# Performance work log

Measured on AMD Instinct MI355X. Metric: run time of the kernel, lower is better.

Reference implementation:

```python
import jax, jax.numpy as jnp
import numpy as np

N = 50000; NE = 250000; NH_EDGES = 125000
DIN = 100; NHID = 100; HEADS = 2; NREL = 500; DREL = 100
ALPHA = 0.2; B = 65536


def l2norm(x, eps=1e-12):
    n = jnp.sqrt(jnp.sum(x * x, axis=1, keepdims=True))
    return x / jnp.maximum(n, eps)


def sp_att(x, edge, edge_embed, a, a2, concat):
    """KBGAT sparse graph attention layer (eval mode, no dropout).
    x: (N, din) node feats; edge: (2, E) int; edge_embed: (E, drel).
    a: (dout, 2*din + drel); a2: (dout,). Aggregates onto edge[0]."""
    din = x.shape[1]
    a_src, a_dst, a_rel = a[:, :din], a[:, din:2 * din], a[:, 2 * din:]
    # edge_m = a @ cat(x[src], x[dst], edge_embed).T, computed without the big concat
    edge_m = x[edge[0]] @ a_src.T + x[edge[1]] @ a_dst.T + edge_embed @ a_rel.T  # (E, dout)
    powers = -jax.nn.leaky_relu(edge_m @ a2, ALPHA)  # (E,)
    edge_e = jnp.exp(powers)
    rowsum = jax.ops.segment_sum(edge_e, edge[0], num_segments=x.shape[0])  # (N,)
    rowsum = jnp.where(rowsum == 0.0, jnp.asarray(1e-12, x.dtype), rowsum)
    h = jax.ops.segment_sum(edge_e[:, None] * edge_m, edge[0], num_segments=x.shape[0])  # (N, dout)
    h = h / rowsum[:, None]
    return jax.nn.elu(h) if concat else h


def setup_inputs() -> dict:
    key = jax.random.key(0)
    ks = jax.random.split(key, 16)
    s1 = np.sqrt(2.0 / (NHID + 2 * DIN + DREL)) * 1.414  # xavier-ish gains
    s2 = np.sqrt(2.0 / (HEADS * NHID + 3 * HEADS * NHID)) * 1.414
    return {
        "entity_embeddings": jax.random.normal(ks[0], (N, DIN), jnp.float32),
        "relation_embeddings": jax.random.normal(ks[1], (NREL, DREL), jnp.float32),
        "entity_rank": jax.random.normal(ks[2], (N,), jnp.float32),
        "a_heads": jax.random.normal(ks[3], (HEADS, NHID, 2 * DIN + DREL), jnp.float32) * s1,
        "a2_heads": jax.random.normal(ks[4], (HEADS, NHID), jnp.float32) * 0.1,
        "W_gat": jax.random.normal(ks[5], (DREL, HEADS * NHID), jnp.float32) * s2,
        "a_out": jax.random.normal(ks[6], (HEADS * NHID, 3 * HEADS * NHID), jnp.float32) * s2,
        "a2_out": jax.random.normal(ks[7], (HEADS * NHID,), jnp.float32) * 0.1,
        "W_entities": jax.random.normal(ks[8], (DIN, HEADS * NHID), jnp.float32) * s2,
        "edge_list": jax.random.randint(ks[9], (2, NE), 0, N, jnp.int32),
        "edge_type": jax.random.randint(ks[10], (NE,), 0, NREL, jnp.int32),
        "train_indices_nhop": jax.random.randint(ks[11], (NH_EDGES, 4), 0, NREL, jnp.int32),
        "batch_inputs": jax.random.randint(ks[12], (B, 3), 0, N, jnp.int32),
    }


def reference(entity_embeddings, relation_embeddings, entity_rank, a_heads, a2_heads,
              W_gat, a_out, a2_out, W_entities, edge_list, edge_type,
              train_indices_nhop, batch_inputs):
    # SpKBGATModified.forward, confidence=False path, eval mode (dropout off).
    x0 = l2norm(entity_embeddings)  # F.normalize(entity_embeddings, p=2, dim=1)
    # 2-hop edges: edge_list_nhop = [nhop[:,3]; nhop[:,0]], edge_type_nhop = nhop[:,1:3]
    edge_list_nhop = jnp.stack([train_indices_nhop[:, 3], train_indices_nhop[:, 0]], axis=0)
    edge_type_nhop = train_indices_nhop[:, 1:3]
    edge = jnp.concatenate([edge_list, edge_list_nhop], axis=1)  # (2, E_total)
    # first-layer edge relation embeddings
    ee1 = jnp.concatenate([
        relation_embeddings[edge_type],
        relation_embeddings[edge_type_nhop[:, 0]] + relation_embeddings[edge_type_nhop[:, 1]],
    ], axis=0)  # (E_total, DREL)
    # multi-head attention, concat heads along feature dim (head0 first, as torch.cat)
    heads = jax.vmap(lambda a, a2: sp_att(x0, edge, ee1, a, a2, True))(a_heads, a2_heads)  # (H, N, NHID)
    x = jnp.transpose(heads, (1, 0, 2)).reshape(x0.shape[0], HEADS * NHID)
    # relation projection and second-hop relation embeddings
    out_relation_1 = relation_embeddings @ W_gat  # (NREL, H*NHID)
    ee2 = jnp.concatenate([
        out_relation_1[edge_type],
        out_relation_1[edge_type_nhop[:, 0]] + out_relation_1[edge_type_nhop[:, 1]],
    ], axis=0)
    x = jax.nn.elu(sp_att(x, edge, ee2, a_out, a2_out, False))  # (N, H*NHID)
    # mask rows touched by batch tails, residual-update and renormalize
    mask = jnp.zeros((x0.shape[0],), x.dtype).at[batch_inputs[:, 2]].set(1.0)
    out_entity_1 = x0 @ W_entities + mask[:, None] * x
    out_entity_1 = l2norm(out_entity_1)
    return out_entity_1, out_relation_1
```

## Files before the change

### kernel.cpp

```cpp
#include <hip/hip_runtime.h>
#include <math.h>

#define NN    50000
#define MP    50048
#define NEDGE 250000
#define NHOPE 125000
#define ETOT  375000
#define NRELS 500
#define BATCH 65536
#define LB1   6250
#define HBMAX 5769

typedef __attribute__((ext_vector_type(8))) short bf16x8;
typedef __attribute__((ext_vector_type(4))) float f32x4;

__device__ __forceinline__ unsigned short bf16rne(float f) {
  unsigned u = __float_as_uint(f);
  unsigned r = (u + 0x7FFFu + ((u >> 16) & 1u)) >> 16;
  return (unsigned short)r;
}
__device__ __forceinline__ float b2f(unsigned short u) {
  return __uint_as_float(((unsigned)u) << 16);
}

struct GJob {
  const unsigned short* A;
  int M;
  const unsigned short* B;
  float* Cf;
  unsigned short* Cbf;
  int ldcb;
  const float* a2;
  float* dot;
  int dotmode;
};

__global__ __launch_bounds__(256) void startk(const float* __restrict__ in,
                                              unsigned short* __restrict__ out,
                                              const int* __restrict__ el, const int* __restrict__ tin,
                                              int* __restrict__ deg) {
  if (blockIdx.y == 1) {
    int i = blockIdx.x * 256 + threadIdx.x;
    if (i < ETOT) {
      int e0 = (i < NEDGE) ? el[i] : tin[(size_t)(i - NEDGE) * 4 + 3];
      atomicAdd(&deg[e0], 1);
    }
    return;
  }
  int row  = blockIdx.x * 4 + (threadIdx.x >> 6);
  int lane = threadIdx.x & 63;
  if (row >= MP) return;
  unsigned short* o = out + (size_t)row * 128;
  if (row >= NN) { o[lane] = 0; o[lane + 64] = 0; return; }
  const float* r = in + (size_t)row * 100;
  float v0 = r[lane];
  float v1 = (lane + 64 < 100) ? r[lane + 64] : 0.f;
  float ss = v0 * v0 + v1 * v1;
  #pragma unroll
  for (int off = 1; off < 64; off <<= 1) ss += __shfl_xor(ss, off);
  float inv = 1.f / fmaxf(sqrtf(ss), 1e-12f);
  o[lane] = bf16rne(v0 * inv);
  o[lane + 64] = (lane + 64 < 100) ? bf16rne(v1 * inv) : (unsigned short)0;
}

template<int KP>
__global__ __launch_bounds__(256) void gemm_multi(GJob j0, GJob j1, GJob j2, GJob j3, GJob j4) {
  __shared__ __attribute__((aligned(16))) char smem[54272];
  unsigned short* shb = (unsigned short*)smem;
  float (*clds)[16][212] = (float (*)[16][212])smem;
  GJob jb = (blockIdx.y == 0) ? j0 : (blockIdx.y == 1) ? j1 : (blockIdx.y == 2) ? j2
          : (blockIdx.y == 3) ? j3 : j4;
  if (blockIdx.x * 64 >= jb.M) return;
  int wv = threadIdx.x >> 6, lane = threadIdx.x & 63;
  int rbw = blockIdx.x * 64 + wv * 16;
  int rl = lane & 15;
  int kq = (lane >> 4) * 8;
  const unsigned short* ap = jb.A + (size_t)(rbw + rl) * KP + kq;
  f32x4 acc[13];
  #pragma unroll
  for (int t = 0; t < 13; ++t) acc[t] = (f32x4){0.f, 0.f, 0.f, 0.f};
  constexpr int NST = (KP + 63) / 64;
  #pragma unroll
  for (int s = 0; s < NST; ++s) {
    const int ks0 = s * 64;
    const int sw  = (KP - ks0 >= 64) ? 64 : (KP - ks0);
    const int cpr = sw / 8;
    __syncthreads();
    for (int idx = threadIdx.x; idx < 208 * cpr; idx += 256) {
      int row = idx / cpr, cw = idx - row * cpr;
      *(float4*)(shb + row * 72 + cw * 8) =
          *(const float4*)(jb.B + (size_t)row * KP + ks0 + cw * 8);
    }
    __syncthreads();
    for (int ksl = 0; ksl < sw; ksl += 32) {
      bf16x8 a0 = *(const bf16x8*)(ap + ks0 + ksl);
      const unsigned short* bl = shb + (size_t)rl * 72 + kq + ksl;
      #pragma unroll
      for (int t = 0; t < 13; ++t) {
        bf16x8 b = *(const bf16x8*)(bl + t * 16 * 72);
        acc[t] = __builtin_amdgcn_mfma_f32_16x16x32_bf16(a0, b, acc[t], 0, 0, 0);
      }
    }
  }
  int rg = (lane >> 4) * 4;
  if (jb.dot) {
    float p0[4] = {0.f, 0.f, 0.f, 0.f}, p1[4] = {0.f, 0.f, 0.f, 0.f};
    #pragma unroll
    for (int t = 0; t < 13; ++t) {
      int col = t * 16 + rl;
      float av = (col < 200) ? jb.a2[col] : 0.f;
      bool lo = (col < 100);
      #pragma unroll
      for (int g = 0; g < 4; ++g) {
        float v = acc[t][g] * av;
        if (lo) p0[g] += v; else p1[g] += v;
      }
    }
    #pragma unroll
    for (int off = 1; off < 16; off <<= 1) {
      #pragma unroll
      for (int g = 0; g < 4; ++g) {
        p0[g] += __shfl_xor(p0[g], off);
        p1[g] += __shfl_xor(p1[g], off);
      }
    }
    if (rl == 0) {
      #pragma unroll
      for (int g = 0; g < 4; ++g) {
        int row = rbw + rg + g;
        if (row < jb.M) {
          if (jb.dotmode == 1) { jb.dot[row * 2] = p0[g]; jb.dot[row * 2 + 1] = p1[g]; }
          else                 { jb.dot[row] = p0[g] + p1[g]; }
        }
      }
    }
  }
  if (jb.Cf || jb.Cbf) {
    __syncthreads();
    #pragma unroll
    for (int t = 0; t < 13; ++t) {
      #pragma unroll
      for (int g = 0; g < 4; ++g)
        clds[wv][rg + g][t * 16 + rl] = acc[t][g];
    }
    __syncthreads();
    #pragma unroll
    for (int i = 0; i < 13; ++i) {
      int idx = i * 64 + lane;
      if (idx < 800) {
        int r = idx / 50, cw = idx - r * 50;
        float4 v = *(const float4*)&clds[wv][r][cw * 4];
        int grow = rbw + r;
        if (grow < jb.M) {
          if (jb.Cf)
            *(float4*)(jb.Cf + (size_t)grow * 200 + cw * 4) = v;
          if (jb.Cbf) {
            ushort4 o = {bf16rne(v.x), bf16rne(v.y), bf16rne(v.z), bf16rne(v.w)};
            *(ushort4*)(jb.Cbf + (size_t)grow * jb.ldcb + cw * 4) = o;
          }
        }
      }
    }
  }
}

__global__ __launch_bounds__(256) void convAll(const float* __restrict__ rel,
                                               const float* __restrict__ ah,
                                               const float* __restrict__ W_ent,
                                               const float* __restrict__ W_gat,
                                               const float* __restrict__ a_out,
                                               unsigned short* __restrict__ B1s,
                                               unsigned short* __restrict__ B1d,
                                               unsigned short* __restrict__ Brel1,
                                               unsigned short* __restrict__ Bxw,
                                               unsigned short* __restrict__ Bwgat,
                                               unsigned short* __restrict__ B2s,
                                               unsigned short* __restrict__ B2d,
                                               unsigned short* __restrict__ B2rel,
                                               unsigned short* __restrict__ relbf) {
  int idx = blockIdx.x * 256 + threadIdx.x;
  int y = blockIdx.y;
  if (y < 3) {
    if (idx >= 208 * 128) return;
    int j = idx >> 7, k = idx & 127;
    float v = 0.f;
    if (j < 200 && k < 100)
      v = ah[((j < 100) ? 0 : 30000) + (j % 100) * 300 + y * 100 + k];
    (y == 0 ? B1s : (y == 1 ? B1d : Brel1))[idx] = bf16rne(v);
  } else if (y == 3) {
    if (idx >= 208 * 128) return;
    int j = idx >> 7, k = idx & 127;
    float v = (j < 200 && k < 100) ? W_ent[(size_t)k * 200 + j] : 0.f;
    Bxw[idx] = bf16rne(v);
  } else if (y == 4) {
    if (idx >= 208 * 128) return;
    int j = idx >> 7, k = idx & 127;
    float v = (j < 200 && k < 100) ? W_gat[(size_t)k * 200 + j] : 0.f;
    Bwgat[idx] = bf16rne(v);
  } else if (y < 8) {
    if (idx >= 208 * 224) return;
    int j = idx / 224, k = idx - j * 224;
    int off = (y - 5) * 200;
    float v = (j < 200 && k < 200) ? a_out[(size_t)j * 600 + off + k] : 0.f;
    (y == 5 ? B2s : (y == 6 ? B2d : B2rel))[idx] = bf16rne(v);
  } else {
    if (idx >= 512 * 128) return;
    int j = idx >> 7, k = idx & 127;
    float v = (j < 500 && k < 100) ? rel[(size_t)j * 100 + k] : 0.f;
    relbf[idx] = bf16rne(v);
  }
}

__global__ __launch_bounds__(256) void scanA(const int* __restrict__ deg, int* __restrict__ bsum, int n) {
  __shared__ int s[256];
  int t = threadIdx.x;
  int i = blockIdx.x * 256 + t;
  s[t] = (i < n) ? deg[i] : 0;
  __syncthreads();
  for (int off = 128; off > 0; off >>= 1) {
    if (t < off) s[t] += s[t + off];
    __syncthreads();
  }
  if (t == 0) bsum[blockIdx.x] = s[0];
}

__global__ __launch_bounds__(256) void scanB(int* __restrict__ bsum, int nb) {
  __shared__ int s[256];
  int t = threadIdx.x;
  int v = (t < nb) ? bsum[t] : 0;
  s[t] = v;
  __syncthreads();
  for (int off = 1; off < 256; off <<= 1) {
    int add = (t >= off) ? s[t - off] : 0;
    __syncthreads();
    s[t] += add;
    __syncthreads();
  }
  if (t < nb) bsum[t] = s[t] - v;
}

__global__ __launch_bounds__(256) void scanC(const int* __restrict__ deg, const int* __restrict__ bsum,
                                             int* __restrict__ offs, int* __restrict__ pos, int n, int total) {
  __shared__ int s[256];
  int t = threadIdx.x;
  int i = blockIdx.x * 256 + t;
  int v = (i < n) ? deg[i] : 0;
  s[t] = v;
  __syncthreads();
  for (int off = 1; off < 256; off <<= 1) {
    int add = (t >= off) ? s[t - off] : 0;
    __syncthreads();
    s[t] += add;
    __syncthreads();
  }
  if (i < n) {
    int e = bsum[blockIdx.x] + s[t] - v;
    offs[i] = e;
    pos[i]  = e;
  }
  if (i == 0) offs[n] = total;
}

__global__ __launch_bounds__(256) void scatBuild(const int* __restrict__ el, const int* __restrict__ et,
                                                 const int* __restrict__ tin, const int* __restrict__ offs,
                                                 int* __restrict__ pos, int2* __restrict__ edata,
                                                 int* __restrict__ lightL, int* __restrict__ heavyL,
                                                 int* __restrict__ cnts) {
  if (blockIdx.y == 0) {
    int i = blockIdx.x * 256 + threadIdx.x;
    if (i >= ETOT) return;
    int e0, e1, t1, t2f;
    if (i < NEDGE) {
      e0 = el[i]; e1 = el[NEDGE + i]; t1 = et[i]; t2f = 0;
    } else {
      const int* q = tin + (size_t)(i - NEDGE) * 4;
      e0 = q[3]; e1 = q[0]; t1 = q[1]; t2f = q[2] + 1;
    }
    int slot = atomicAdd(&pos[e0], 1);
    edata[slot] = make_int2(e1 | (t1 << 16), t2f | (e0 << 9));
    return;
  }
  int i = blockIdx.x * 256 + threadIdx.x;
  int lane = threadIdx.x & 63;
  bool valid = (i < NN);
  int d = valid ? (offs[i + 1] - offs[i]) : 0;
  bool heavy = valid && (d > 64);
  bool light = valid && (d <= 64);
  unsigned long long mh = __ballot(heavy);
  unsigned long long ml = __ballot(light);
  unsigned long long below = (1ULL << lane) - 1ULL;
  int bh = 0, bl = 0;
  if (lane == 0) {
    if (mh) bh = atomicAdd(&cnts[1], __popcll(mh));
    if (ml) bl = atomicAdd(&cnts[0], __popcll(ml));
  }
  bh = __shfl(bh, 0);
  bl = __shfl(bl, 0);
  if (heavy) heavyL[bh + __popcll(mh & below)] = i;
  if (light) lightL[bl + __popcll(ml & below)] = i;
}

__global__ __launch_bounds__(256) void eeMisc1(const int2* __restrict__ edata,
                                               const float* __restrict__ ssrc,
                                               const float* __restrict__ sdst,
                                               const float* __restrict__ srel,
                                               float2* __restrict__ ee,
                                               unsigned short* __restrict__ xbf,
                                               const int* __restrict__ bi,
                                               float* __restrict__ maskA) {
  if (blockIdx.y == 1) {
    if (blockIdx.x < 42) {
      int i = blockIdx.x * 256 + threadIdx.x;
      if (i < (MP - NN) * 224) xbf[(size_t)NN * 224 + i] = 0;
    } else if (blockIdx.x < 42 + 256) {
      int t = (blockIdx.x - 42) * 256 + threadIdx.x;
      if (t < BATCH) maskA[bi[t * 3 + 2]] = 1.0f;
    }
    return;
  }
  int q = blockIdx.x * 256 + threadIdx.x;
  if (q >= ETOT) return;
  int2 ed = edata[q];
  int e1 = ed.x & 0xFFFF;
  int t1 = ((unsigned)ed.x) >> 16;
  int t2f = ed.y & 0x1FF;
  int e0 = ((unsigned)ed.y) >> 9;
  float p0 = ssrc[e0 * 2]     + sdst[e1 * 2]     + srel[t1 * 2];
  float p1 = ssrc[e0 * 2 + 1] + sdst[e1 * 2 + 1] + srel[t1 * 2 + 1];
  if (t2f) { int t2 = t2f - 1; p0 += srel[t2 * 2]; p1 += srel[t2 * 2 + 1]; }
  p0 = (p0 > 0.f) ? p0 : 0.2f * p0;
  p1 = (p1 > 0.f) ? p1 : 0.2f * p1;
  ee[q] = make_float2(__expf(-p0), __expf(-p1));
}

__global__ __launch_bounds__(256) void edgeEE2(const int2* __restrict__ edata,
                                               const float* __restrict__ ssrc,
                                               const float* __restrict__ sdst,
                                               const float* __restrict__ srel,
                                               float* __restrict__ ee) {
  int q = blockIdx.x * 256 + threadIdx.x;
  if (q >= ETOT) return;
  int2 ed = edata[q];
  int e1 = ed.x & 0xFFFF;
  int t1 = ((unsigned)ed.x) >> 16;
  int t2f = ed.y & 0x1FF;
  int e0 = ((unsigned)ed.y) >> 9;
  float p = ssrc[e0] + sdst[e1] + srel[t1];
  if (t2f) p += srel[t2f - 1];
  p = (p > 0.f) ? p : 0.2f * p;
  ee[q] = __expf(-p);
}

__global__ __launch_bounds__(512) void gather1M(const int* __restrict__ lightL, const int* __restrict__ heavyL,
    const int* __restrict__ cnts, const int* __restrict__ offs, const int2* __restrict__ edata,
    const float2* __restrict__ eeb,
    const unsigned short* __restrict__ srcb, const unsigned short* __restrict__ dstb,
    const unsigned short* __restrict__ relpb,
    unsigned short* __restrict__ xbf) {
  __shared__ float part[8][208];
  int w = threadIdx.x >> 6, lane = threadIdx.x & 63;
  bool act = lane < 50;
  int cb = lane * 4;
  float a0 = 0.f, a1 = 0.f, a2v = 0.f, a3 = 0.f, rs0 = 0.f, rs1 = 0.f;
  bool hd0 = (cb < 100);
  auto edgeop = [&](int2 ed, float2 ev) {
    int e1 = ed.x & 0xFFFF;
    int t1 = ((unsigned)ed.x) >> 16;
    int t2f = ed.y & 0x1FF;
    rs0 += ev.x; rs1 += ev.y;
    if (act) {
      ushort4 dv = *(const ushort4*)(dstb + (size_t)e1 * 200 + cb);
      ushort4 rv = *(const ushort4*)(relpb + (size_t)t1 * 200 + cb);
      float m0 = b2f(dv.x) + b2f(rv.x);
      float m1 = b2f(dv.y) + b2f(rv.y);
      float m2 = b2f(dv.z) + b2f(rv.z);
      float m3 = b2f(dv.w) + b2f(rv.w);
      if (t2f) {
        ushort4 r2 = *(const ushort4*)(relpb + (size_t)(t2f - 1) * 200 + cb);
        m0 += b2f(r2.x); m1 += b2f(r2.y); m2 += b2f(r2.z); m3 += b2f(r2.w);
      }
      float ee = hd0 ? ev.x : ev.y;
      a0 += ee * m0; a1 += ee * m1; a2v += ee * m2; a3 += ee * m3;
    }
  };
  if (blockIdx.x < HBMAX) {
    int hidx = blockIdx.x;
    if (hidx >= cnts[1]) return;
    int node = heavyL[hidx];
    int s = offs[node], e = offs[node + 1];
    int q = s + w;
    for (; q + 8 < e; q += 16) { edgeop(edata[q], eeb[q]); edgeop(edata[q + 8], eeb[q + 8]); }
    if (q < e) edgeop(edata[q], eeb[q]);
    if (act) { part[w][cb] = a0; part[w][cb + 1] = a1; part[w][cb + 2] = a2v; part[w][cb + 3] = a3; }
    if (lane == 0) { part[w][200] = rs0; part[w][201] = rs1; }
    __syncthreads();
    int t = threadIdx.x;
    if (t < 224) {
      unsigned short outv = 0;
      if (t < 200) {
        float a = 0.f, r0 = 0.f, r1 = 0.f;
        #pragma unroll
        for (int wv = 0; wv < 8; ++wv) { a += part[wv][t]; r0 += part[wv][200]; r1 += part[wv][201]; }
        float inv = (t < 100) ? 1.f / r0 : 1.f / r1;
        float v = b2f(srcb[(size_t)node * 200 + t]) + a * inv;
        v = (v > 0.f) ? v : expm1f(v);
        outv = bf16rne(v);
      }
      xbf[(size_t)node * 224 + t] = outv;
    }
    return;
  }
  int widx = (blockIdx.x - HBMAX) * 8 + w;
  if (widx >= cnts[0]) return;
  int node = lightL[widx];
  int s = offs[node], e = offs[node + 1];
  int q = s;
  for (; q + 1 < e; q += 2) { edgeop(edata[q], eeb[q]); edgeop(edata[q + 1], eeb[q + 1]); }
  if (q < e) edgeop(edata[q], eeb[q]);
  bool has = (e > s);
  unsigned short* xo = xbf + (size_t)node * 224;
  if (act) {
    float inv = has ? (hd0 ? 1.f / rs0 : 1.f / rs1) : 0.f;
    ushort4 sv = *(const ushort4*)(srcb + (size_t)node * 200 + cb);
    float v0 = has ? b2f(sv.x) + a0 * inv : 0.f;
    float v1 = has ? b2f(sv.y) + a1 * inv : 0.f;
    float v2 = has ? b2f(sv.z) + a2v * inv : 0.f;
    float v3 = has ? b2f(sv.w) + a3 * inv : 0.f;
    v0 = (v0 > 0.f) ? v0 : expm1f(v0);
    v1 = (v1 > 0.f) ? v1 : expm1f(v1);
    v2 = (v2 > 0.f) ? v2 : expm1f(v2);
    v3 = (v3 > 0.f) ? v3 : expm1f(v3);
    ushort4 ov = {bf16rne(v0), bf16rne(v1), bf16rne(v2), bf16rne(v3)};
    *(ushort4*)(xo + cb) = ov;
  } else if (lane < 56) {
    ushort4 z = {0, 0, 0, 0};
    *(ushort4*)(xo + cb) = z;
  }
}

__global__ __launch_bounds__(512) void gather2M(const int* __restrict__ lightL, const int* __restrict__ heavyL,
    const int* __restrict__ cnts, const int* __restrict__ offs, const int2* __restrict__ edata,
    const float* __restrict__ eeb,
    const unsigned short* __restrict__ srcb, const unsigned short* __restrict__ dstb,
    const unsigned short* __restrict__ relpb,
    unsigned short* __restrict__ h2b) {
  __shared__ float part[8][208];
  int w = threadIdx.x >> 6, lane = threadIdx.x & 63;
  bool act = lane < 50;
  int cb = lane * 4;
  float a0 = 0.f, a1 = 0.f, a2v = 0.f, a3 = 0.f, rs = 0.f;
  auto edgeop = [&](int2 ed, float ee) {
    int e1 = ed.x & 0xFFFF;
    int t1 = ((unsigned)ed.x) >> 16;
    int t2f = ed.y & 0x1FF;
    rs += ee;
    if (act) {
      ushort4 dv = *(const ushort4*)(dstb + (size_t)e1 * 200 + cb);
      ushort4 rv = *(const ushort4*)(relpb + (size_t)t1 * 200 + cb);
      float m0 = b2f(dv.x) + b2f(rv.x);
      float m1 = b2f(dv.y) + b2f(rv.y);
      float m2 = b2f(dv.z) + b2f(rv.z);
      float m3 = b2f(dv.w) + b2f(rv.w);
      if (t2f) {
        ushort4 r2 = *(const ushort4*)(relpb + (size_t)(t2f - 1) * 200 + cb);
        m0 += b2f(r2.x); m1 += b2f(r2.y); m2 += b2f(r2.z); m3 += b2f(r2.w);
      }
      a0 += ee * m0; a1 += ee * m1; a2v += ee * m2; a3 += ee * m3;
    }
  };
  if (blockIdx.x < HBMAX) {
    int hidx = blockIdx.x;
    if (hidx >= cnts[1]) return;
    int node = heavyL[hidx];
    int s = offs[node], e = offs[node + 1];
    int q = s + w;
    for (; q + 8 < e; q += 16) { edgeop(edata[q], eeb[q]); edgeop(edata[q + 8], eeb[q + 8]); }
    if (q < e) edgeop(edata[q], eeb[q]);
    if (act) { part[w][cb] = a0; part[w][cb + 1] = a1; part[w][cb + 2] = a2v; part[w][cb + 3] = a3; }
    if (lane == 0) part[w][200] = rs;
    __syncthreads();
    int t = threadIdx.x;
    if (t < 200) {
      float a = 0.f, r = 0.f;
      #pragma unroll
      for (int wv = 0; wv < 8; ++wv) { a += part[wv][t]; r += part[wv][200]; }
      float v = b2f(srcb[(size_t)node * 200 + t]) + a / r;
      v = (v > 0.f) ? v : expm1f(v);
      h2b[(size_t)node * 200 + t] = bf16rne(v);
    }
    return;
  }
  int widx = (blockIdx.x - HBMAX) * 8 + w;
  if (widx >= cnts[0]) return;
  int node = lightL[widx];
  int s = offs[node], e = offs[node + 1];
  int q = s;
  for (; q + 1 < e; q += 2) { edgeop(edata[q], eeb[q]); edgeop(edata[q + 1], eeb[q + 1]); }
  if (q < e) edgeop(edata[q], eeb[q]);
  if (!act) return;
  bool has = (e > s);
  float inv = has ? 1.f / rs : 0.f;
  ushort4 sv = *(const ushort4*)(srcb + (size_t)node * 200 + cb);
  float v0 = has ? b2f(sv.x) + a0 * inv : 0.f;
  float v1 = has ? b2f(sv.y) + a1 * inv : 0.f;
  float v2 = has ? b2f(sv.z) + a2v * inv : 0.f;
  float v3 = has ? b2f(sv.w) + a3 * inv : 0.f;
  v0 = (v0 > 0.f) ? v0 : expm1f(v0);
  v1 = (v1 > 0.f) ? v1 : expm1f(v1);
  v2 = (v2 > 0.f) ? v2 : expm1f(v2);
  v3 = (v3 > 0.f) ? v3 : expm1f(v3);
  ushort4 ov = {bf16rne(v0), bf16rne(v1), bf16rne(v2), bf16rne(v3)};
  *(ushort4*)(h2b + (size_t)node * 200 + cb) = ov;
}

__global__ __launch_bounds__(256) void finalk2(const float* __restrict__ xw,
                                               const unsigned short* __restrict__ h2b,
                                               const float* __restrict__ maskA, float* __restrict__ out) {
  int row  = blockIdx.x * 4 + (threadIdx.x >> 6);
  int lane = threadIdx.x & 63;
  if (row >= NN) return;
  bool act = lane < 50;
  int cb = lane * 4;
  float m = maskA[row];
  float v0 = 0.f, v1 = 0.f, v2 = 0.f, v3 = 0.f;
  if (act) {
    float4 xv = *(const float4*)(xw + (size_t)row * 200 + cb);
    ushort4 hv = *(const ushort4*)(h2b + (size_t)row * 200 + cb);
    v0 = xv.x + m * b2f(hv.x);
    v1 = xv.y + m * b2f(hv.y);
    v2 = xv.z + m * b2f(hv.z);
    v3 = xv.w + m * b2f(hv.w);
  }
  float ss = v0 * v0 + v1 * v1 + v2 * v2 + v3 * v3;
  #pragma unroll
  for (int off = 1; off < 64; off <<= 1) ss += __shfl_xor(ss, off);
  float inv = 1.f / fmaxf(sqrtf(ss), 1e-12f);
  if (act) {
    float4 ov = {v0 * inv, v1 * inv, v2 * inv, v3 * inv};
    *(float4*)(out + (size_t)row * 200 + cb) = ov;
  }
}

extern "C" void kernel_launch(void* const* d_in, const int* in_sizes, int n_in,
                              void* d_out, int out_size, void* d_ws, size_t ws_size,
                              hipStream_t stream) {
  (void)in_sizes; (void)n_in; (void)out_size; (void)ws_size;
  const float* ent      = (const float*)d_in[0];
  const float* rel      = (const float*)d_in[1];
  const float* a_heads  = (const float*)d_in[3];
  const float* a2_heads = (const float*)d_in[4];
  const float* W_gat    = (const float*)d_in[5];
  const float* a_out    = (const float*)d_in[6];
  const float* a2_out   = (const float*)d_in[7];
  const float* W_ent    = (const float*)d_in[8];
  const int* edge_list  = (const int*)d_in[9];
  const int* edge_type  = (const int*)d_in[10];
  const int* tin        = (const int*)d_in[11];
  const int* binp       = (const int*)d_in[12];

  float* out    = (float*)d_out;
  float* outrel = out + 10000000;

  float* ws = (float*)d_ws;
  unsigned short* bufSb  = (unsigned short*)ws;
  unsigned short* dstD   = (unsigned short*)(ws + 5000000);
  unsigned short* relp1b = (unsigned short*)(ws + 10000000);
  unsigned short* relp2b = (unsigned short*)(ws + 10050000);
  float* ssrc1 = ws + 10100000;
  float* sdst1 = ws + 10200000;
  float* s2src = ws + 10300000;
  float* s2dst = ws + 10350000;
  float* srel1 = ws + 10400000;
  float* s2rel = ws + 10402000;
  float* maskA = ws + 10404000;
  unsigned short* h2b   = (unsigned short*)(ws + 10460000);
  unsigned short* x0nbf = (unsigned short*)(ws + 15460000);
  unsigned short* xbf   = (unsigned short*)(ws + 18700000);
  unsigned short* B1s   = (unsigned short*)(ws + 24310000);
  unsigned short* B1d   = (unsigned short*)(ws + 24325000);
  unsigned short* Brel1 = (unsigned short*)(ws + 24340000);
  unsigned short* Bxw   = (unsigned short*)(ws + 24355000);
  unsigned short* Bwgat = (unsigned short*)(ws + 24370000);
  unsigned short* B2s   = (unsigned short*)(ws + 24385000);
  unsigned short* B2d   = (unsigned short*)(ws + 24410000);
  unsigned short* B2rel = (unsigned short*)(ws + 24435000);
  unsigned short* relbf = (unsigned short*)(ws + 24460000);
  unsigned short* orelb = (unsigned short*)(ws + 24495000);
  float2* eeb1 = (float2*)(ws + 24555000);
  float*  eeb2 = ws + 25305000;
  int* ibase  = (int*)(ws + 25700000);
  int* deg    = ibase;
  int* offs   = ibase + 50000;
  int* pos    = ibase + 100016;
  int* bsum   = ibase + 150016;
  int* cnts   = ibase + 150272;
  int* lightL = ibase + 150280;
  int* heavyL = ibase + 200280;
  int2* edata = (int2*)(ibase + 250288);

  hipMemsetAsync(deg,   0, (size_t)NN * 4, stream);
  hipMemsetAsync(maskA, 0, (size_t)NN * 4, stream);
  hipMemsetAsync(cnts,  0, 8, stream);
  hipMemsetAsync(orelb, 0, (size_t)512 * 224 * 2, stream);

  {
    dim3 g(12512, 2);
    startk<<<g, 256, 0, stream>>>(ent, x0nbf, edge_list, tin, deg);
  }
  scanA<<<196, 256, 0, stream>>>(deg, bsum, NN);
  scanB<<<1, 256, 0, stream>>>(bsum, 196);
  scanC<<<196, 256, 0, stream>>>(deg, bsum, offs, pos, NN, ETOT);
  {
    dim3 g(1465, 2);
    scatBuild<<<g, 256, 0, stream>>>(edge_list, edge_type, tin, offs, pos, edata,
                                     lightL, heavyL, cnts);
  }
  {
    dim3 g(256, 9);
    convAll<<<g, 256, 0, stream>>>(rel, a_heads, W_ent, W_gat, a_out,
                                   B1s, B1d, Brel1, Bxw, Bwgat, B2s, B2d, B2rel, relbf);
  }

  {
    GJob js    = {x0nbf, NN,    B1s,   nullptr, bufSb,  200, a2_heads, ssrc1, 1};
    GJob jd    = {x0nbf, NN,    B1d,   nullptr, dstD,   200, a2_heads, sdst1, 1};
    GJob jx    = {x0nbf, NN,    Bxw,   out,     nullptr, 0,  nullptr,  nullptr, 0};
    GJob jrel1 = {relbf, NRELS, Brel1, nullptr, relp1b, 200, a2_heads, srel1, 1};
    GJob jorel = {relbf, NRELS, Bwgat, outrel,  orelb,  224, nullptr,  nullptr, 0};
    dim3 g(782, 5);
    gemm_multi<128><<<g, 256, 0, stream>>>(js, jd, jx, jrel1, jorel);
  }

  {
    dim3 g(1465, 2);
    eeMisc1<<<g, 256, 0, stream>>>(edata, ssrc1, sdst1, srel1, eeb1, xbf, binp, maskA);
  }

  gather1M<<<HBMAX + LB1, 512, 0, stream>>>(lightL, heavyL, cnts, offs, edata, eeb1,
                                            bufSb, dstD, relp1b, xbf);

  {
    GJob js    = {xbf,   NN,    B2s,   nullptr, bufSb,  200, a2_out, s2src, 2};
    GJob jd    = {xbf,   NN,    B2d,   nullptr, dstD,   200, a2_out, s2dst, 2};
    GJob jrp2  = {orelb, NRELS, B2rel, nullptr, relp2b, 200, a2_out, s2rel, 2};
    GJob jz    = {nullptr, 0, nullptr, nullptr, nullptr, 0, nullptr, nullptr, 0};
    dim3 g(782, 3);
    gemm_multi<224><<<g, 256, 0, stream>>>(js, jd, jrp2, jz, jz);
  }

  edgeEE2<<<(ETOT + 255) / 256, 256, 0, stream>>>(edata, s2src, s2dst, s2rel, eeb2);

  gather2M<<<HBMAX + LB1, 512, 0, stream>>>(lightL, heavyL, cnts, offs, edata, eeb2,
                                            bufSb, dstD, relp2b, h2b);

  finalk2<<<12500, 256, 0, stream>>>(out, h2b, maskA, out);
}
```

Before: 390.2 us.

## Fuse weight conversion, scan stages, and final normalize into neighboring kernels

```diff
diff --git a/kernel.cpp b/kernel.cpp
--- a/kernel.cpp
+++ b/kernel.cpp
@@ -38,12 +38,60 @@
 __global__ __launch_bounds__(256) void startk(const float* __restrict__ in,
                                               unsigned short* __restrict__ out,
                                               const int* __restrict__ el, const int* __restrict__ tin,
-                                              int* __restrict__ deg) {
+                                              int* __restrict__ deg,
+                                              const float* __restrict__ rel,
+                                              const float* __restrict__ ah,
+                                              const float* __restrict__ W_ent,
+                                              const float* __restrict__ W_gat,
+                                              const float* __restrict__ a_out,
+                                              unsigned short* __restrict__ B1s,
+                                              unsigned short* __restrict__ B1d,
+                                              unsigned short* __restrict__ Brel1,
+                                              unsigned short* __restrict__ Bxw,
+                                              unsigned short* __restrict__ Bwgat,
+                                              unsigned short* __restrict__ B2s,
+                                              unsigned short* __restrict__ B2d,
+                                              unsigned short* __restrict__ B2rel,
+                                              unsigned short* __restrict__ relbf) {
   if (blockIdx.y == 1) {
     int i = blockIdx.x * 256 + threadIdx.x;
     if (i < ETOT) {
       int e0 = (i < NEDGE) ? el[i] : tin[(size_t)(i - NEDGE) * 4 + 3];
       atomicAdd(&deg[e0], 1);
+    }
+    return;
+  }
+  if (blockIdx.y == 2) {
+    const int S1 = 26624, S2 = 46592;
+    int idx = blockIdx.x * 256 + threadIdx.x;
+    if (idx < 3 * S1) {
+      int y = idx / S1, r = idx - y * S1;
+      int j = r >> 7, k = r & 127;
+      float v = 0.f;
+      if (j < 200 && k < 100)
+        v = ah[((j < 100) ? 0 : 30000) + (j % 100) * 300 + y * 100 + k];
+      (y == 0 ? B1s : (y == 1 ? B1d : Brel1))[r] = bf16rne(v);
+    } else if (idx < 4 * S1) {
+      int r = idx - 3 * S1;
+      int j = r >> 7, k = r & 127;
+      float v = (j < 200 && k < 100) ? W_ent[(size_t)k * 200 + j] : 0.f;
+      Bxw[r] = bf16rne(v);
+    } else if (idx < 5 * S1) {
+      int r = idx - 4 * S1;
+      int j = r >> 7, k = r & 127;
+      float v = (j < 200 && k < 100) ? W_gat[(size_t)k * 200 + j] : 0.f;
+      Bwgat[r] = bf16rne(v);
+    } else if (idx < 5 * S1 + 3 * S2) {
+      int r = idx - 5 * S1;
+      int y = r / S2; r -= y * S2;
+      int j = r / 224, k = r - j * 224;
+      float v = (j < 200 && k < 200) ? a_out[(size_t)j * 600 + y * 200 + k] : 0.f;
+      (y == 0 ? B2s : (y == 1 ? B2d : B2rel))[r] = bf16rne(v);
+    } else if (idx < 5 * S1 + 3 * S2 + 65536) {
+      int r = idx - 5 * S1 - 3 * S2;
+      int j = r >> 7, k = r & 127;
+      float v = (j < 500 && k < 100) ? rel[(size_t)j * 100 + k] : 0.f;
+      relbf[r] = bf16rne(v);
     }
     return;
   }
@@ -164,53 +212,6 @@
   }
 }
 
-__global__ __launch_bounds__(256) void convAll(const float* __restrict__ rel,
-                                               const float* __restrict__ ah,
-                                               const float* __restrict__ W_ent,
-                                               const float* __restrict__ W_gat,
-                                               const float* __restrict__ a_out,
-                                               unsigned short* __restrict__ B1s,
-                                               unsigned short* __restrict__ B1d,
-                                               unsigned short* __restrict__ Brel1,
-                                               unsigned short* __restrict__ Bxw,
-                                               unsigned short* __restrict__ Bwgat,
-                                               unsigned short* __restrict__ B2s,
-                                               unsigned short* __restrict__ B2d,
-                                               unsigned short* __restrict__ B2rel,
-                                               unsigned short* __restrict__ relbf) {
-  int idx = blockIdx.x * 256 + threadIdx.x;
-  int y = blockIdx.y;
-  if (y < 3) {
-    if (idx >= 208 * 128) return;
-    int j = idx >> 7, k = idx & 127;
-    float v = 0.f;
-    if (j < 200 && k < 100)
-      v = ah[((j < 100) ? 0 : 30000) + (j % 100) * 300 + y * 100 + k];
-    (y == 0 ? B1s : (y == 1 ? B1d : Brel1))[idx] = bf16rne(v);
-  } else if (y == 3) {
-    if (idx >= 208 * 128) return;
-    int j = idx >> 7, k = idx & 127;
-    float v = (j < 200 && k < 100) ? W_ent[(size_t)k * 200 + j] : 0.f;
-    Bxw[idx] = bf16rne(v);
-  } else if (y == 4) {
-    if (idx >= 208 * 128) return;
-    int j = idx >> 7, k = idx & 127;
-    float v = (j < 200 && k < 100) ? W_gat[(size_t)k * 200 + j] : 0.f;
-    Bwgat[idx] = bf16rne(v);
-  } else if (y < 8) {
-    if (idx >= 208 * 224) return;
-    int j = idx / 224, k = idx - j * 224;
-    int off = (y - 5) * 200;
-    float v = (j < 200 && k < 200) ? a_out[(size_t)j * 600 + off + k] : 0.f;
-    (y == 5 ? B2s : (y == 6 ? B2d : B2rel))[idx] = bf16rne(v);
-  } else {
-    if (idx >= 512 * 128) return;
-    int j = idx >> 7, k = idx & 127;
-    float v = (j < 500 && k < 100) ? rel[(size_t)j * 100 + k] : 0.f;
-    relbf[idx] = bf16rne(v);
-  }
-}
-
 __global__ __launch_bounds__(256) void scanA(const int* __restrict__ deg, int* __restrict__ bsum, int n) {
   __shared__ int s[256];
   int t = threadIdx.x;
@@ -224,25 +225,20 @@
   if (t == 0) bsum[blockIdx.x] = s[0];
 }
 
-__global__ __launch_bounds__(256) void scanB(int* __restrict__ bsum, int nb) {
+__global__ __launch_bounds__(256) void scanC(const int* __restrict__ deg, const int* __restrict__ bsum,
+                                             int* __restrict__ offs, int* __restrict__ pos, int n, int total) {
+  __shared__ int sb[256];
   __shared__ int s[256];
   int t = threadIdx.x;
-  int v = (t < nb) ? bsum[t] : 0;
-  s[t] = v;
+  sb[t] = (t < 196) ? bsum[t] : 0;
   __syncthreads();
   for (int off = 1; off < 256; off <<= 1) {
-    int add = (t >= off) ? s[t - off] : 0;
-    __syncthreads();
-    s[t] += add;
-    __syncthreads();
-  }
-  if (t < nb) bsum[t] = s[t] - v;
-}
-
-__global__ __launch_bounds__(256) void scanC(const int* __restrict__ deg, const int* __restrict__ bsum,
-                                             int* __restrict__ offs, int* __restrict__ pos, int n, int total) {
-  __shared__ int s[256];
-  int t = threadIdx.x;
+    int add = (t >= off) ? sb[t - off] : 0;
+    __syncthreads();
+    sb[t] += add;
+    __syncthreads();
+  }
+  int base = (blockIdx.x == 0) ? 0 : sb[blockIdx.x - 1];
   int i = blockIdx.x * 256 + t;
   int v = (i < n) ? deg[i] : 0;
   s[t] = v;
@@ -254,7 +250,7 @@
     __syncthreads();
   }
   if (i < n) {
-    int e = bsum[blockIdx.x] + s[t] - v;
+    int e = base + s[t] - v;
     offs[i] = e;
     pos[i]  = e;
   }
@@ -443,8 +439,9 @@
     const float* __restrict__ eeb,
     const unsigned short* __restrict__ srcb, const unsigned short* __restrict__ dstb,
     const unsigned short* __restrict__ relpb,
-    unsigned short* __restrict__ h2b) {
+    const float* __restrict__ maskA, float* __restrict__ out) {
   __shared__ float part[8][208];
+  __shared__ float red[512];
   int w = threadIdx.x >> 6, lane = threadIdx.x & 63;
   bool act = lane < 50;
   int cb = lane * 4;
@@ -480,14 +477,25 @@
     if (lane == 0) part[w][200] = rs;
     __syncthreads();
     int t = threadIdx.x;
+    float m = maskA[node];
+    float u = 0.f;
     if (t < 200) {
       float a = 0.f, r = 0.f;
       #pragma unroll
       for (int wv = 0; wv < 8; ++wv) { a += part[wv][t]; r += part[wv][200]; }
       float v = b2f(srcb[(size_t)node * 200 + t]) + a / r;
       v = (v > 0.f) ? v : expm1f(v);
-      h2b[(size_t)node * 200 + t] = bf16rne(v);
-    }
+      u = out[(size_t)node * 200 + t] + m * v;
+    }
+    red[t] = u * u;
+    __syncthreads();
+    #pragma unroll
+    for (int off = 256; off > 0; off >>= 1) {
+      if (t < off) red[t] += red[t + off];
+      __syncthreads();
+    }
+    float inv = 1.f / fmaxf(sqrtf(red[0]), 1e-12f);
+    if (t < 200) out[(size_t)node * 200 + t] = u * inv;
     return;
   }
   int widx = (blockIdx.x - HBMAX) * 8 + w;
@@ -497,47 +505,33 @@
   int q = s;
   for (; q + 1 < e; q += 2) { edgeop(edata[q], eeb[q]); edgeop(edata[q + 1], eeb[q + 1]); }
   if (q < e) edgeop(edata[q], eeb[q]);
-  if (!act) return;
   bool has = (e > s);
-  float inv = has ? 1.f / rs : 0.f;
-  ushort4 sv = *(const ushort4*)(srcb + (size_t)node * 200 + cb);
-  float v0 = has ? b2f(sv.x) + a0 * inv : 0.f;
-  float v1 = has ? b2f(sv.y) + a1 * inv : 0.f;
-  float v2 = has ? b2f(sv.z) + a2v * inv : 0.f;
-  float v3 = has ? b2f(sv.w) + a3 * inv : 0.f;
-  v0 = (v0 > 0.f) ? v0 : expm1f(v0);
-  v1 = (v1 > 0.f) ? v1 : expm1f(v1);
-  v2 = (v2 > 0.f) ? v2 : expm1f(v2);
-  v3 = (v3 > 0.f) ? v3 : expm1f(v3);
-  ushort4 ov = {bf16rne(v0), bf16rne(v1), bf16rne(v2), bf16rne(v3)};
-  *(ushort4*)(h2b + (size_t)node * 200 + cb) = ov;
-}
-
-__global__ __launch_bounds__(256) void finalk2(const float* __restrict__ xw,
-                                               const unsigned short* __restrict__ h2b,
-                                               const float* __restrict__ maskA, float* __restrict__ out) {
-  int row  = blockIdx.x * 4 + (threadIdx.x >> 6);
-  int lane = threadIdx.x & 63;
-  if (row >= NN) return;
-  bool act = lane < 50;
-  int cb = lane * 4;
-  float m = maskA[row];
-  float v0 = 0.f, v1 = 0.f, v2 = 0.f, v3 = 0.f;
+  float m = maskA[node];
+  float u0 = 0.f, u1 = 0.f, u2 = 0.f, u3 = 0.f;
   if (act) {
-    float4 xv = *(const float4*)(xw + (size_t)row * 200 + cb);
-    ushort4 hv = *(const ushort4*)(h2b + (size_t)row * 200 + cb);
-    v0 = xv.x + m * b2f(hv.x);
-    v1 = xv.y + m * b2f(hv.y);
-    v2 = xv.z + m * b2f(hv.z);
-    v3 = xv.w + m * b2f(hv.w);
-  }
-  float ss = v0 * v0 + v1 * v1 + v2 * v2 + v3 * v3;
+    float inv = has ? 1.f / rs : 0.f;
+    ushort4 sv = *(const ushort4*)(srcb + (size_t)node * 200 + cb);
+    float v0 = has ? b2f(sv.x) + a0 * inv : 0.f;
+    float v1 = has ? b2f(sv.y) + a1 * inv : 0.f;
+    float v2 = has ? b2f(sv.z) + a2v * inv : 0.f;
+    float v3 = has ? b2f(sv.w) + a3 * inv : 0.f;
+    v0 = (v0 > 0.f) ? v0 : expm1f(v0);
+    v1 = (v1 > 0.f) ? v1 : expm1f(v1);
+    v2 = (v2 > 0.f) ? v2 : expm1f(v2);
+    v3 = (v3 > 0.f) ? v3 : expm1f(v3);
+    float4 xv = *(const float4*)(out + (size_t)node * 200 + cb);
+    u0 = xv.x + m * v0;
+    u1 = xv.y + m * v1;
+    u2 = xv.z + m * v2;
+    u3 = xv.w + m * v3;
+  }
+  float ss = u0 * u0 + u1 * u1 + u2 * u2 + u3 * u3;
   #pragma unroll
   for (int off = 1; off < 64; off <<= 1) ss += __shfl_xor(ss, off);
   float inv = 1.f / fmaxf(sqrtf(ss), 1e-12f);
   if (act) {
-    float4 ov = {v0 * inv, v1 * inv, v2 * inv, v3 * inv};
-    *(float4*)(out + (size_t)row * 200 + cb) = ov;
+    float4 ov = {u0 * inv, u1 * inv, u2 * inv, u3 * inv};
+    *(float4*)(out + (size_t)node * 200 + cb) = ov;
   }
 }
 
@@ -573,52 +567,44 @@
   float* srel1 = ws + 10400000;
   float* s2rel = ws + 10402000;
   float* maskA = ws + 10404000;
-  unsigned short* h2b   = (unsigned short*)(ws + 10460000);
-  unsigned short* x0nbf = (unsigned short*)(ws + 15460000);
-  unsigned short* xbf   = (unsigned short*)(ws + 18700000);
-  unsigned short* B1s   = (unsigned short*)(ws + 24310000);
-  unsigned short* B1d   = (unsigned short*)(ws + 24325000);
-  unsigned short* Brel1 = (unsigned short*)(ws + 24340000);
-  unsigned short* Bxw   = (unsigned short*)(ws + 24355000);
-  unsigned short* Bwgat = (unsigned short*)(ws + 24370000);
-  unsigned short* B2s   = (unsigned short*)(ws + 24385000);
-  unsigned short* B2d   = (unsigned short*)(ws + 24410000);
-  unsigned short* B2rel = (unsigned short*)(ws + 24435000);
-  unsigned short* relbf = (unsigned short*)(ws + 24460000);
-  unsigned short* orelb = (unsigned short*)(ws + 24495000);
-  float2* eeb1 = (float2*)(ws + 24555000);
-  float*  eeb2 = ws + 25305000;
-  int* ibase  = (int*)(ws + 25700000);
-  int* deg    = ibase;
-  int* offs   = ibase + 50000;
-  int* pos    = ibase + 100016;
-  int* bsum   = ibase + 150016;
-  int* cnts   = ibase + 150272;
-  int* lightL = ibase + 150280;
-  int* heavyL = ibase + 200280;
-  int2* edata = (int2*)(ibase + 250288);
-
-  hipMemsetAsync(deg,   0, (size_t)NN * 4, stream);
-  hipMemsetAsync(maskA, 0, (size_t)NN * 4, stream);
-  hipMemsetAsync(cnts,  0, 8, stream);
-  hipMemsetAsync(orelb, 0, (size_t)512 * 224 * 2, stream);
+  int*   deg   = (int*)(ws + 10454000);
+  int*   cnts  = (int*)(ws + 10504000);
+  unsigned short* orelb = (unsigned short*)(ws + 10504008);
+  unsigned short* x0nbf = (unsigned short*)(ws + 10570000);
+  unsigned short* xbf   = (unsigned short*)(ws + 13780000);
+  unsigned short* B1s   = (unsigned short*)(ws + 19390000);
+  unsigned short* B1d   = (unsigned short*)(ws + 19405000);
+  unsigned short* Brel1 = (unsigned short*)(ws + 19420000);
+  unsigned short* Bxw   = (unsigned short*)(ws + 19435000);
+  unsigned short* Bwgat = (unsigned short*)(ws + 19450000);
+  unsigned short* B2s   = (unsigned short*)(ws + 19465000);
+  unsigned short* B2d   = (unsigned short*)(ws + 19490000);
+  unsigned short* B2rel = (unsigned short*)(ws + 19515000);
+  unsigned short* relbf = (unsigned short*)(ws + 19540000);
+  float2* eeb1 = (float2*)(ws + 19580000);
+  float*  eeb2 = ws + 20330000;
+  int* ibase  = (int*)(ws + 20710000);
+  int* offs   = ibase;
+  int* pos    = ibase + 50016;
+  int* bsum   = ibase + 100016;
+  int* lightL = ibase + 100288;
+  int* heavyL = ibase + 150288;
+  int2* edata = (int2*)(ibase + 200288);
+
+  hipMemsetAsync(maskA, 0, (size_t)(10561352 - 10404000) * 4, stream);
 
   {
-    dim3 g(12512, 2);
-    startk<<<g, 256, 0, stream>>>(ent, x0nbf, edge_list, tin, deg);
+    dim3 g(12512, 3);
+    startk<<<g, 256, 0, stream>>>(ent, x0nbf, edge_list, tin, deg,
+                                  rel, a_heads, W_ent, W_gat, a_out,
+                                  B1s, B1d, Brel1, Bxw, Bwgat, B2s, B2d, B2rel, relbf);
   }
   scanA<<<196, 256, 0, stream>>>(deg, bsum, NN);
-  scanB<<<1, 256, 0, stream>>>(bsum, 196);
   scanC<<<196, 256, 0, stream>>>(deg, bsum, offs, pos, NN, ETOT);
   {
     dim3 g(1465, 2);
     scatBuild<<<g, 256, 0, stream>>>(edge_list, edge_type, tin, offs, pos, edata,
                                      lightL, heavyL, cnts);
-  }
-  {
-    dim3 g(256, 9);
-    convAll<<<g, 256, 0, stream>>>(rel, a_heads, W_ent, W_gat, a_out,
-                                   B1s, B1d, Brel1, Bxw, Bwgat, B2s, B2d, B2rel, relbf);
   }
 
   {
@@ -651,7 +637,5 @@
   edgeEE2<<<(ETOT + 255) / 256, 256, 0, stream>>>(edata, s2src, s2dst, s2rel, eeb2);
 
   gather2M<<<HBMAX + LB1, 512, 0, stream>>>(lightL, heavyL, cnts, offs, edata, eeb2,
-                                            bufSb, dstD, relp2b, h2b);
-
-  finalk2<<<12500, 256, 0, stream>>>(out, h2b, maskA, out);
-}
+                                            bufSb, dstD, relp2b, maskA, out);
+}
```

Result: faster. 369.9 us (-5.2%).
